# Kernel optimization log

Hardware: AMD Instinct MI355X
Metric: run time of the kernel (lower is better)

The kernel has to match this reference:

```python
import jax, jax.numpy as jnp
import numpy as np

B, L, DK, DV, H = 2, 2048, 512, 512, 8
DH_K = DK // H  # 64
DH_V = DV // H  # 64


def setup_inputs() -> dict:
    key = jax.random.key(0)
    ks = jax.random.split(key, 6)
    scale_w = 1.0 / np.sqrt(DK)
    return {
        "keys": jax.random.normal(ks[0], (B, L, DK), dtype=jnp.float32),
        "queries": jax.random.normal(ks[1], (B, L, DK), dtype=jnp.float32),
        "values": jax.random.normal(ks[2], (B, L, DV), dtype=jnp.float32),
        "WQ": jax.random.normal(ks[3], (H, DK, DH_K), dtype=jnp.float32) * scale_w,
        "WK": jax.random.normal(ks[4], (H, DK, DH_K), dtype=jnp.float32) * scale_w,
        "WV": jax.random.normal(ks[5], (H, DV, DH_V), dtype=jnp.float32) * scale_w,
    }


def reference(keys, queries, values, WQ, WK, WV):
    # Per-head projections, vectorized over all H heads at once.
    Q = jnp.einsum('bld,hde->bhle', queries, WQ)   # [B,H,Lq,dh]
    K = jnp.einsum('bld,hde->bhle', keys, WK)      # [B,H,Lk,dh]
    V = jnp.einsum('bld,hde->bhle', values, WV)    # [B,H,Lk,dv_h]
    Lk = keys.shape[1]
    # NOTE: original scales by sqrt(seq_len_k), not sqrt(head_dim).
    y = jnp.einsum('bhqe,bhke->bhqk', Q, K) / jnp.sqrt(jnp.float32(Lk))
    # NOTE: original applies softmax over torch dim=1 of [B,Lq,Lk],
    # i.e. the QUERY axis (axis=2 here in [B,H,Lq,Lk]).
    z = jax.nn.softmax(y, axis=2)
    out = jnp.einsum('bhqk,bhke->bhqe', z, V)      # [B,H,Lq,dv_h]
    # Concat heads on the feature dim (same order as torch.concat(..., 2)).
    Bq, Hh, Lq, Dh = out.shape
    return out.transpose(0, 2, 1, 3).reshape(Bq, Lq, Hh * Dh)
```

## Files before the change

kernel.cpp:

```cpp
#include <hip/hip_runtime.h>
#include <hip/hip_bf16.h>

#define LL 2048
#define DM 512
#define SCALE2 0.031879357f

typedef unsigned short u16;
typedef __attribute__((ext_vector_type(8))) short short8;
typedef __attribute__((ext_vector_type(4))) short short4v;
typedef __attribute__((ext_vector_type(4))) float f32x4;

#define XAQ_OFF 0u
#define XAK_OFF 2097152u
#define XAV_OFF 4194304u
#define WB_OFF  6291456u
#define QA_OFF  7077888u
#define KA_OFF  9175040u
#define VB_OFF  11272192u
#define S_OFF   13369344u

__device__ __forceinline__ u16 f2bf(float f) {
  union { float f; unsigned u; } v; v.f = f;
  unsigned r = v.u + 0x7fff + ((v.u >> 16) & 1);
  return (u16)(r >> 16);
}
__device__ __forceinline__ size_t frag_idx(int bh, int t64, int w, int c, int lane) {
  return ((((size_t)(bh * 32 + t64) * 4 + w) * 2 + c) * 64 + lane) * 8;
}
__device__ __forceinline__ size_t vb8_idx(int bh, int kt2, int w, int et, int lane) {
  return ((((size_t)(bh * 16 + kt2) * 4 + w) * 4 + et) * 64 + lane) * 8;
}

__global__ __launch_bounds__(256) void prep_kernel(
    const float* __restrict__ queries, const float* __restrict__ keys,
    const float* __restrict__ values, const float* __restrict__ WQ,
    const float* __restrict__ WK, const float* __restrict__ WV,
    u16* __restrict__ wsb) {
  int t = threadIdx.x;
  int blk = blockIdx.x;
  if (blk < 768) {
    int tens = blk >> 8;
    int grp  = blk & 255;
    const float* src = (tens == 0 ? queries : tens == 1 ? keys : values) +
                       (size_t)grp * 16 * 512;
    __shared__ __align__(16) u16 Xs[16][520];
#pragma unroll
    for (int rep = 0; rep < 8; ++rep) {
      int f4 = t + rep * 256;
      int row = f4 >> 7, c4 = f4 & 127;
      float4 v = *(const float4*)(src + (size_t)row * 512 + c4 * 4);
      short4v o;
      o[0] = (short)f2bf(v.x); o[1] = (short)f2bf(v.y);
      o[2] = (short)f2bf(v.z); o[3] = (short)f2bf(v.w);
      *(short4v*)&Xs[row][c4 * 4] = o;
    }
    __syncthreads();
    u16* dst = wsb + (tens == 0 ? XAQ_OFF : tens == 1 ? XAK_OFF : XAV_OFF) +
               (size_t)grp * 16 * 64 * 8;
#pragma unroll
    for (int rep = 0; rep < 4; ++rep) {
      int o = t + rep * 256;
      int kt = o >> 6, lane = o & 63;
      int quad = lane >> 4, l16 = lane & 15;
      short8 v = *(const short8*)&Xs[l16][kt * 32 + quad * 8];
      *(short8*)(dst + (size_t)o * 8) = v;
    }
  } else {
    int c2 = (blk - 768) * 256 + t;
    int lane = c2 & 63;
    int nt = (c2 >> 6) & 3;
    int kt = (c2 >> 8) & 15;
    int h  = (c2 >> 12) & 7;
    int z  = c2 >> 15;
    int quad = lane >> 4, l16 = lane & 15;
    const float* W = (z == 0) ? WQ : (z == 1) ? WK : WV;
    const float* src = W + ((size_t)h * DM + kt * 32 + quad * 8) * 64 + nt * 16 + l16;
    short8 o;
#pragma unroll
    for (int j = 0; j < 8; ++j) o[j] = (short)f2bf(src[(size_t)j * 64]);
    *(short8*)(wsb + WB_OFF + (size_t)c2 * 8) = o;
  }
}

__global__ __launch_bounds__(256) void proj_kernel(u16* __restrict__ wsb) {
  int t = threadIdx.x;
  int lane = t & 63, w = t >> 6, quad = lane >> 4, l16 = lane & 15;
  int z = blockIdx.z, bh = blockIdx.y, b = bh >> 3, h = bh & 7;
  int QT = blockIdx.x;

  const u16* Bw = wsb + WB_OFF + ((size_t)(z * 8 + h) * 16) * 4 * 64 * 8;
  const u16* Ab = wsb + (z == 0 ? XAQ_OFF : z == 1 ? XAK_OFF : XAV_OFF) +
      (((size_t)b * 128 + QT * 4 + w) * 16) * 64 * 8;

  f32x4 acc[4];
#pragma unroll
  for (int nt = 0; nt < 4; ++nt) acc[nt] = (f32x4){0.f, 0.f, 0.f, 0.f};

#pragma unroll 4
  for (int kt = 0; kt < 16; ++kt) {
    short8 a = *(const short8*)(Ab + ((size_t)kt * 64 + lane) * 8);
#pragma unroll
    for (int nt = 0; nt < 4; ++nt) {
      short8 bb = *(const short8*)(Bw + (((size_t)kt * 4 + nt) * 64 + lane) * 8);
      acc[nt] = __builtin_amdgcn_mfma_f32_16x16x32_bf16(a, bb, acc[nt], 0, 0, 0);
    }
  }

  __shared__ float Cs[64][68];
  float sc = (z == 0) ? SCALE2 : 1.0f;
#pragma unroll
  for (int nt = 0; nt < 4; ++nt)
#pragma unroll
    for (int r = 0; r < 4; ++r)
      Cs[w * 16 + quad * 4 + r][nt * 16 + l16] = acc[nt][r] * sc;
  __syncthreads();

  if (z < 2) {
    u16* base = wsb + (z == 0 ? QA_OFF : KA_OFF);
#pragma unroll
    for (int c = 0; c < 2; ++c) {
      const float* srcr = &Cs[w * 16 + l16][c * 32 + quad * 8];
      short8 o;
#pragma unroll
      for (int j = 0; j < 8; ++j) o[j] = (short)f2bf(srcr[j]);
      *(short8*)(base + frag_idx(bh, QT, w, c, lane)) = o;
    }
  } else {
#pragma unroll
    for (int et = 0; et < 4; ++et) {
      short4v o;
#pragma unroll
      for (int j = 0; j < 4; ++j)
        o[j] = (short)f2bf(Cs[w * 16 + quad * 4 + j][et * 16 + l16]);
      *(short4v*)(wsb + VB_OFF + vb8_idx(bh, QT >> 1, w, et, lane) + (QT & 1) * 4) = o;
    }
  }
}

__global__ __launch_bounds__(256) void stats_kernel(u16* __restrict__ wsb) {
  int t = threadIdx.x;
  int lane = t & 63, w = t >> 6, quad = lane >> 4, l16 = lane & 15;
  int bh = blockIdx.x;
  int KT = blockIdx.y;

  short8 ka[4][2];
#pragma unroll
  for (int mt = 0; mt < 4; ++mt)
#pragma unroll
    for (int c = 0; c < 2; ++c)
      ka[mt][c] = *(const short8*)(wsb + KA_OFF + frag_idx(bh, KT, mt, c, lane));

  float rs[4][4];
#pragma unroll
  for (int mt = 0; mt < 4; ++mt)
#pragma unroll
    for (int r = 0; r < 4; ++r) rs[mt][r] = 0.f;

  short8 qb0 = *(const short8*)(wsb + QA_OFF + frag_idx(bh, 0, w, 0, lane));
  short8 qb1 = *(const short8*)(wsb + QA_OFF + frag_idx(bh, 0, w, 1, lane));
  for (int qt = 0; qt < 32; ++qt) {
    int qn = (qt + 1) & 31;
    short8 nq0 = *(const short8*)(wsb + QA_OFF + frag_idx(bh, qn, w, 0, lane));
    short8 nq1 = *(const short8*)(wsb + QA_OFF + frag_idx(bh, qn, w, 1, lane));
#pragma unroll
    for (int mt = 0; mt < 4; ++mt) {
      f32x4 y = (f32x4){0.f, 0.f, 0.f, 0.f};
      __builtin_amdgcn_s_setprio(1);
      y = __builtin_amdgcn_mfma_f32_16x16x32_bf16(ka[mt][0], qb0, y, 0, 0, 0);
      y = __builtin_amdgcn_mfma_f32_16x16x32_bf16(ka[mt][1], qb1, y, 0, 0, 0);
      __builtin_amdgcn_s_setprio(0);
#pragma unroll
      for (int r = 0; r < 4; ++r) rs[mt][r] += __builtin_amdgcn_exp2f(y[r]);
    }
    qb0 = nq0; qb1 = nq1;
  }
#pragma unroll
  for (int mt = 0; mt < 4; ++mt)
#pragma unroll
    for (int r = 0; r < 4; ++r) {
      rs[mt][r] += __shfl_xor(rs[mt][r], 1);
      rs[mt][r] += __shfl_xor(rs[mt][r], 2);
      rs[mt][r] += __shfl_xor(rs[mt][r], 4);
      rs[mt][r] += __shfl_xor(rs[mt][r], 8);
    }

  __shared__ float Sred[4][64];
  if (l16 == 0) {
#pragma unroll
    for (int mt = 0; mt < 4; ++mt)
#pragma unroll
      for (int r = 0; r < 4; ++r)
        Sred[w][mt * 16 + quad * 4 + r] = rs[mt][r];
  }
  __syncthreads();
  if (t < 64) {
    float s = Sred[0][t] + Sred[1][t] + Sred[2][t] + Sred[3][t];
    float* S = (float*)(wsb + S_OFF);
    S[(size_t)bh * LL + KT * 64 + t] = 1.0f / s;
  }
}

__global__ __launch_bounds__(256, 2) void attn_kernel(const u16* __restrict__ wsb,
                                                      float* __restrict__ out) {
  int t = threadIdx.x;
  int lane = t & 63, w = t >> 6, quad = lane >> 4, l16 = lane & 15;
  int bh = blockIdx.x, b = bh >> 3, h = bh & 7;
  int QT = blockIdx.y, qbase = QT * 64;
  const float* S = (const float*)(wsb + S_OFF) + (size_t)bh * LL;

  short8 qf[4][2];
#pragma unroll
  for (int nt = 0; nt < 4; ++nt)
#pragma unroll
    for (int c = 0; c < 2; ++c)
      qf[nt][c] = *(const short8*)(wsb + QA_OFF + frag_idx(bh, QT, nt, c, lane));

  f32x4 oacc[4][4];
#pragma unroll
  for (int nt = 0; nt < 4; ++nt)
#pragma unroll
    for (int et = 0; et < 4; ++et) oacc[nt][et] = (f32x4){0.f, 0.f, 0.f, 0.f};

  short8 kae0 = *(const short8*)(wsb + KA_OFF + frag_idx(bh, 0, w, 0, lane));
  short8 kae1 = *(const short8*)(wsb + KA_OFF + frag_idx(bh, 0, w, 1, lane));
  short8 kao0 = *(const short8*)(wsb + KA_OFF + frag_idx(bh, 1, w, 0, lane));
  short8 kao1 = *(const short8*)(wsb + KA_OFF + frag_idx(bh, 1, w, 1, lane));
  short8 vb8[4];
#pragma unroll
  for (int et = 0; et < 4; ++et)
    vb8[et] = *(const short8*)(wsb + VB_OFF + vb8_idx(bh, 0, w, et, lane));
  float4 s4e = *(const float4*)(S + 0 * 64 + w * 16 + quad * 4);
  float4 s4o = *(const float4*)(S + 1 * 64 + w * 16 + quad * 4);

  for (int kt2 = 0; kt2 < 16; ++kt2) {
    int kne = (2 * kt2 + 2) & 31, kno = (2 * kt2 + 3) & 31;
    int k2n = (kt2 + 1) & 15;
    short8 nkae0 = *(const short8*)(wsb + KA_OFF + frag_idx(bh, kne, w, 0, lane));
    short8 nkae1 = *(const short8*)(wsb + KA_OFF + frag_idx(bh, kne, w, 1, lane));
    short8 nkao0 = *(const short8*)(wsb + KA_OFF + frag_idx(bh, kno, w, 0, lane));
    short8 nkao1 = *(const short8*)(wsb + KA_OFF + frag_idx(bh, kno, w, 1, lane));
    short8 nvb8[4];
#pragma unroll
    for (int et = 0; et < 4; ++et)
      nvb8[et] = *(const short8*)(wsb + VB_OFF + vb8_idx(bh, k2n, w, et, lane));
    float4 ns4e = *(const float4*)(S + kne * 64 + w * 16 + quad * 4);
    float4 ns4o = *(const float4*)(S + kno * 64 + w * 16 + quad * 4);

#pragma unroll
    for (int nt = 0; nt < 4; ++nt) {
      f32x4 ye = (f32x4){0.f, 0.f, 0.f, 0.f};
      f32x4 yo = (f32x4){0.f, 0.f, 0.f, 0.f};
      __builtin_amdgcn_s_setprio(1);
      ye = __builtin_amdgcn_mfma_f32_16x16x32_bf16(kae0, qf[nt][0], ye, 0, 0, 0);
      ye = __builtin_amdgcn_mfma_f32_16x16x32_bf16(kae1, qf[nt][1], ye, 0, 0, 0);
      yo = __builtin_amdgcn_mfma_f32_16x16x32_bf16(kao0, qf[nt][0], yo, 0, 0, 0);
      yo = __builtin_amdgcn_mfma_f32_16x16x32_bf16(kao1, qf[nt][1], yo, 0, 0, 0);
      __builtin_amdgcn_s_setprio(0);
      short8 pa8;
      pa8[0] = (short)f2bf(__builtin_amdgcn_exp2f(ye[0]) * s4e.x);
      pa8[1] = (short)f2bf(__builtin_amdgcn_exp2f(ye[1]) * s4e.y);
      pa8[2] = (short)f2bf(__builtin_amdgcn_exp2f(ye[2]) * s4e.z);
      pa8[3] = (short)f2bf(__builtin_amdgcn_exp2f(ye[3]) * s4e.w);
      pa8[4] = (short)f2bf(__builtin_amdgcn_exp2f(yo[0]) * s4o.x);
      pa8[5] = (short)f2bf(__builtin_amdgcn_exp2f(yo[1]) * s4o.y);
      pa8[6] = (short)f2bf(__builtin_amdgcn_exp2f(yo[2]) * s4o.z);
      pa8[7] = (short)f2bf(__builtin_amdgcn_exp2f(yo[3]) * s4o.w);
      __builtin_amdgcn_s_setprio(1);
#pragma unroll
      for (int et = 0; et < 4; ++et)
        oacc[nt][et] = __builtin_amdgcn_mfma_f32_16x16x32_bf16(pa8, vb8[et], oacc[nt][et], 0, 0, 0);
      __builtin_amdgcn_s_setprio(0);
    }
    kae0 = nkae0; kae1 = nkae1; kao0 = nkao0; kao1 = nkao1;
#pragma unroll
    for (int et = 0; et < 4; ++et) vb8[et] = nvb8[et];
    s4e = ns4e; s4o = ns4o;
  }

  __shared__ float red[4][64][68];
#pragma unroll
  for (int nt = 0; nt < 4; ++nt)
#pragma unroll
    for (int et = 0; et < 4; ++et)
#pragma unroll
      for (int r = 0; r < 4; ++r)
        red[w][nt * 16 + quad * 4 + r][et * 16 + l16] = oacc[nt][et][r];
  __syncthreads();
  float* og = out + ((size_t)b * LL + qbase + w * 16) * 512 + h * 64;
#pragma unroll
  for (int i = 0; i < 16; ++i) {
    float s = red[0][w * 16 + i][lane] + red[1][w * 16 + i][lane] +
              red[2][w * 16 + i][lane] + red[3][w * 16 + i][lane];
    og[(size_t)i * 512 + lane] = s;
  }
}

extern "C" void kernel_launch(void* const* d_in, const int* in_sizes, int n_in,
                              void* d_out, int out_size, void* d_ws, size_t ws_size,
                              hipStream_t stream) {
  const float* keys    = (const float*)d_in[0];
  const float* queries = (const float*)d_in[1];
  const float* values  = (const float*)d_in[2];
  const float* WQ      = (const float*)d_in[3];
  const float* WK      = (const float*)d_in[4];
  const float* WV      = (const float*)d_in[5];
  float* out = (float*)d_out;
  u16* wsb = (u16*)d_ws;

  prep_kernel<<<dim3(1152), 256, 0, stream>>>(queries, keys, values, WQ, WK, WV, wsb);
  proj_kernel<<<dim3(32, 16, 3), 256, 0, stream>>>(wsb);
  stats_kernel<<<dim3(16, 32), 256, 0, stream>>>(wsb);
  attn_kernel<<<dim3(16, 32), 256, 0, stream>>>(wsb, out);
}
```

Before: 135.4 us.

## Fuse four stage kernels into one cooperative kernel with grid syncs

Merges the prep, projection, stats and attention kernels into a single persistent cooperative kernel of 512 blocks, separated by grid-wide barriers. Shared memory is one union reused across stages. The goal is to remove three kernel launch boundaries and their gaps. In exchange, the kernel is limited to 512 resident blocks, projection loops over three z per block, and prep is strided. The union is sized by the largest stage buffer, which may lower occupancy. The old four-launch path stays as a fallback if the cooperative launch fails.

Measured after the change: 468.0 us. +245.5%, slower.

```diff
diff --git a/kernel.cpp b/kernel.cpp
--- a/kernel.cpp
+++ b/kernel.cpp
@@ -1,5 +1,8 @@
 #include <hip/hip_runtime.h>
 #include <hip/hip_bf16.h>
+#include <hip/hip_cooperative_groups.h>
+
+namespace cg = cooperative_groups;
 
 #define LL 2048
 #define DM 512
@@ -31,19 +34,18 @@
   return ((((size_t)(bh * 16 + kt2) * 4 + w) * 4 + et) * 64 + lane) * 8;
 }
 
-__global__ __launch_bounds__(256) void prep_kernel(
+
+__device__ __forceinline__ void prep_body(
+    int vb, int t, u16* Xs ,
     const float* __restrict__ queries, const float* __restrict__ keys,
     const float* __restrict__ values, const float* __restrict__ WQ,
     const float* __restrict__ WK, const float* __restrict__ WV,
     u16* __restrict__ wsb) {
-  int t = threadIdx.x;
-  int blk = blockIdx.x;
-  if (blk < 768) {
-    int tens = blk >> 8;
-    int grp  = blk & 255;
+  if (vb < 768) {
+    int tens = vb >> 8;
+    int grp  = vb & 255;
     const float* src = (tens == 0 ? queries : tens == 1 ? keys : values) +
                        (size_t)grp * 16 * 512;
-    __shared__ __align__(16) u16 Xs[16][520];
 #pragma unroll
     for (int rep = 0; rep < 8; ++rep) {
       int f4 = t + rep * 256;
@@ -52,7 +54,7 @@
       short4v o;
       o[0] = (short)f2bf(v.x); o[1] = (short)f2bf(v.y);
       o[2] = (short)f2bf(v.z); o[3] = (short)f2bf(v.w);
-      *(short4v*)&Xs[row][c4 * 4] = o;
+      *(short4v*)&Xs[row * 520 + c4 * 4] = o;
     }
     __syncthreads();
     u16* dst = wsb + (tens == 0 ? XAQ_OFF : tens == 1 ? XAK_OFF : XAV_OFF) +
@@ -62,11 +64,12 @@
       int o = t + rep * 256;
       int kt = o >> 6, lane = o & 63;
       int quad = lane >> 4, l16 = lane & 15;
-      short8 v = *(const short8*)&Xs[l16][kt * 32 + quad * 8];
+      short8 v = *(const short8*)&Xs[l16 * 520 + kt * 32 + quad * 8];
       *(short8*)(dst + (size_t)o * 8) = v;
     }
+    __syncthreads();
   } else {
-    int c2 = (blk - 768) * 256 + t;
+    int c2 = (vb - 768) * 256 + t;
     int lane = c2 & 63;
     int nt = (c2 >> 6) & 3;
     int kt = (c2 >> 8) & 15;
@@ -82,11 +85,10 @@
   }
 }
 
-__global__ __launch_bounds__(256) void proj_kernel(u16* __restrict__ wsb) {
-  int t = threadIdx.x;
+__device__ __forceinline__ void proj_body(
+    int z, int bh, int QT, int t, float* Cs , u16* __restrict__ wsb) {
   int lane = t & 63, w = t >> 6, quad = lane >> 4, l16 = lane & 15;
-  int z = blockIdx.z, bh = blockIdx.y, b = bh >> 3, h = bh & 7;
-  int QT = blockIdx.x;
+  int b = bh >> 3, h = bh & 7;
 
   const u16* Bw = wsb + WB_OFF + ((size_t)(z * 8 + h) * 16) * 4 * 64 * 8;
   const u16* Ab = wsb + (z == 0 ? XAQ_OFF : z == 1 ? XAK_OFF : XAV_OFF) +
@@ -106,20 +108,19 @@
     }
   }
 
-  __shared__ float Cs[64][68];
   float sc = (z == 0) ? SCALE2 : 1.0f;
 #pragma unroll
   for (int nt = 0; nt < 4; ++nt)
 #pragma unroll
     for (int r = 0; r < 4; ++r)
-      Cs[w * 16 + quad * 4 + r][nt * 16 + l16] = acc[nt][r] * sc;
+      Cs[(w * 16 + quad * 4 + r) * 68 + nt * 16 + l16] = acc[nt][r] * sc;
   __syncthreads();
 
   if (z < 2) {
     u16* base = wsb + (z == 0 ? QA_OFF : KA_OFF);
 #pragma unroll
     for (int c = 0; c < 2; ++c) {
-      const float* srcr = &Cs[w * 16 + l16][c * 32 + quad * 8];
+      const float* srcr = &Cs[(w * 16 + l16) * 68 + c * 32 + quad * 8];
       short8 o;
 #pragma unroll
       for (int j = 0; j < 8; ++j) o[j] = (short)f2bf(srcr[j]);
@@ -131,17 +132,16 @@
       short4v o;
 #pragma unroll
       for (int j = 0; j < 4; ++j)
-        o[j] = (short)f2bf(Cs[w * 16 + quad * 4 + j][et * 16 + l16]);
+        o[j] = (short)f2bf(Cs[(w * 16 + quad * 4 + j) * 68 + et * 16 + l16]);
       *(short4v*)(wsb + VB_OFF + vb8_idx(bh, QT >> 1, w, et, lane) + (QT & 1) * 4) = o;
     }
   }
-}
-
-__global__ __launch_bounds__(256) void stats_kernel(u16* __restrict__ wsb) {
-  int t = threadIdx.x;
+  __syncthreads();
+}
+
+__device__ __forceinline__ void stats_body(
+    int bh, int KT, int t, float* Sred , u16* __restrict__ wsb) {
   int lane = t & 63, w = t >> 6, quad = lane >> 4, l16 = lane & 15;
-  int bh = blockIdx.x;
-  int KT = blockIdx.y;
 
   short8 ka[4][2];
 #pragma unroll
@@ -184,28 +184,28 @@
       rs[mt][r] += __shfl_xor(rs[mt][r], 8);
     }
 
-  __shared__ float Sred[4][64];
   if (l16 == 0) {
 #pragma unroll
     for (int mt = 0; mt < 4; ++mt)
 #pragma unroll
       for (int r = 0; r < 4; ++r)
-        Sred[w][mt * 16 + quad * 4 + r] = rs[mt][r];
+        Sred[w * 64 + mt * 16 + quad * 4 + r] = rs[mt][r];
   }
   __syncthreads();
   if (t < 64) {
-    float s = Sred[0][t] + Sred[1][t] + Sred[2][t] + Sred[3][t];
+    float s = Sred[0 * 64 + t] + Sred[1 * 64 + t] + Sred[2 * 64 + t] + Sred[3 * 64 + t];
     float* S = (float*)(wsb + S_OFF);
     S[(size_t)bh * LL + KT * 64 + t] = 1.0f / s;
   }
-}
-
-__global__ __launch_bounds__(256, 2) void attn_kernel(const u16* __restrict__ wsb,
-                                                      float* __restrict__ out) {
-  int t = threadIdx.x;
+  __syncthreads();
+}
+
+__device__ __forceinline__ void attn_body(
+    int bh, int QT, int t, float* red ,
+    const u16* __restrict__ wsb, float* __restrict__ out) {
   int lane = t & 63, w = t >> 6, quad = lane >> 4, l16 = lane & 15;
-  int bh = blockIdx.x, b = bh >> 3, h = bh & 7;
-  int QT = blockIdx.y, qbase = QT * 64;
+  int b = bh >> 3, h = bh & 7;
+  int qbase = QT * 64;
   const float* S = (const float*)(wsb + S_OFF) + (size_t)bh * LL;
 
   short8 qf[4][2];
@@ -277,22 +277,78 @@
     s4e = ns4e; s4o = ns4o;
   }
 
-  __shared__ float red[4][64][68];
 #pragma unroll
   for (int nt = 0; nt < 4; ++nt)
 #pragma unroll
     for (int et = 0; et < 4; ++et)
 #pragma unroll
       for (int r = 0; r < 4; ++r)
-        red[w][nt * 16 + quad * 4 + r][et * 16 + l16] = oacc[nt][et][r];
+        red[(w * 64 + nt * 16 + quad * 4 + r) * 68 + et * 16 + l16] = oacc[nt][et][r];
   __syncthreads();
   float* og = out + ((size_t)b * LL + qbase + w * 16) * 512 + h * 64;
 #pragma unroll
   for (int i = 0; i < 16; ++i) {
-    float s = red[0][w * 16 + i][lane] + red[1][w * 16 + i][lane] +
-              red[2][w * 16 + i][lane] + red[3][w * 16 + i][lane];
+    int row = w * 16 + i;
+    float s = red[(0 * 64 + row) * 68 + lane] + red[(1 * 64 + row) * 68 + lane] +
+              red[(2 * 64 + row) * 68 + lane] + red[(3 * 64 + row) * 68 + lane];
     og[(size_t)i * 512 + lane] = s;
   }
+}
+
+__global__ __launch_bounds__(256, 2) void fused_kernel(
+    const float* __restrict__ queries, const float* __restrict__ keys,
+    const float* __restrict__ values, const float* __restrict__ WQ,
+    const float* __restrict__ WK, const float* __restrict__ WV,
+    u16* __restrict__ wsb, float* __restrict__ out) {
+  __shared__ __align__(16) union {
+    u16   Xs[16 * 520];
+    float Cs[64 * 68];
+    float Sred[4 * 64];
+    float red[4 * 64 * 68];
+  } sm;
+  cg::grid_group grid = cg::this_grid();
+  int t = threadIdx.x;
+  int blk = blockIdx.x;
+  int bh = blk & 15, QT = blk >> 4;
+
+  for (int vb = blk; vb < 1152; vb += 512)
+    prep_body(vb, t, sm.Xs, queries, keys, values, WQ, WK, WV, wsb);
+  __threadfence();
+  grid.sync();
+
+#pragma unroll 1
+  for (int z = 0; z < 3; ++z)
+    proj_body(z, bh, QT, t, sm.Cs, wsb);
+  __threadfence();
+  grid.sync();
+
+  stats_body(bh, QT, t, sm.Sred, wsb);
+  __threadfence();
+  grid.sync();
+
+  attn_body(bh, QT, t, sm.red, wsb, out);
+}
+
+__global__ __launch_bounds__(256) void prep_kernel(
+    const float* __restrict__ queries, const float* __restrict__ keys,
+    const float* __restrict__ values, const float* __restrict__ WQ,
+    const float* __restrict__ WK, const float* __restrict__ WV,
+    u16* __restrict__ wsb) {
+  __shared__ __align__(16) u16 Xs[16 * 520];
+  prep_body(blockIdx.x, threadIdx.x, Xs, queries, keys, values, WQ, WK, WV, wsb);
+}
+__global__ __launch_bounds__(256) void proj_kernel(u16* __restrict__ wsb) {
+  __shared__ float Cs[64 * 68];
+  proj_body(blockIdx.z, blockIdx.y, blockIdx.x, threadIdx.x, Cs, wsb);
+}
+__global__ __launch_bounds__(256) void stats_kernel(u16* __restrict__ wsb) {
+  __shared__ float Sred[4 * 64];
+  stats_body(blockIdx.x, blockIdx.y, threadIdx.x, Sred, wsb);
+}
+__global__ __launch_bounds__(256, 2) void attn_kernel(const u16* __restrict__ wsb,
+                                                      float* __restrict__ out) {
+  __shared__ float red[4 * 64 * 68];
+  attn_body(blockIdx.x, blockIdx.y, threadIdx.x, red, wsb, out);
 }
 
 extern "C" void kernel_launch(void* const* d_in, const int* in_sizes, int n_in,
@@ -307,8 +363,14 @@
   float* out = (float*)d_out;
   u16* wsb = (u16*)d_ws;
 
-  prep_kernel<<<dim3(1152), 256, 0, stream>>>(queries, keys, values, WQ, WK, WV, wsb);
-  proj_kernel<<<dim3(32, 16, 3), 256, 0, stream>>>(wsb);
-  stats_kernel<<<dim3(16, 32), 256, 0, stream>>>(wsb);
-  attn_kernel<<<dim3(16, 32), 256, 0, stream>>>(wsb, out);
-}
+  void* args[] = {(void*)&queries, (void*)&keys, (void*)&values,
+                  (void*)&WQ, (void*)&WK, (void*)&WV, (void*)&wsb, (void*)&out};
+  hipError_t err = hipLaunchCooperativeKernel((const void*)fused_kernel,
+                                              dim3(512), dim3(256), args, 0, stream);
+  if (err != hipSuccess) {
+    prep_kernel<<<dim3(1152), 256, 0, stream>>>(queries, keys, values, WQ, WK, WV, wsb);
+    proj_kernel<<<dim3(32, 16, 3), 256, 0, stream>>>(wsb);
+    stats_kernel<<<dim3(16, 32), 256, 0, stream>>>(wsb);
+    attn_kernel<<<dim3(16, 32), 256, 0, stream>>>(wsb, out);
+  }
+}
```
